# Performance work log

Measured on AMD Instinct MI355X. Metric: run time of the kernel, lower is better.

## Reference

```python
import jax, jax.numpy as jnp
import numpy as np

N_NODES = 100000
N_EDGES = 1600000
D = 128
R = 3
L = 3


def setup_inputs() -> dict:
    key = jax.random.key(0)
    ks = jax.random.split(key, 6)
    features = jax.random.normal(ks[0], (N_NODES, D), dtype=jnp.float32)
    # per-layer relation weights [L, R, D, D], self-loop weights [L, D, D], bias [L, D]
    W = jax.random.normal(ks[1], (L, R, D, D), dtype=jnp.float32) * 0.05
    W_self = jax.random.normal(ks[2], (L, D, D), dtype=jnp.float32) * 0.05
    bias = jnp.zeros((L, D), dtype=jnp.float32)
    src = jax.random.randint(ks[3], (N_EDGES,), 0, N_NODES, dtype=jnp.int32)
    dst = jax.random.randint(ks[4], (N_EDGES,), 0, N_NODES, dtype=jnp.int32)
    etypes = jax.random.randint(ks[5], (N_EDGES,), 0, R, dtype=jnp.int32)
    return {"features": features, "W": W, "W_self": W_self, "bias": bias,
            "src": src, "dst": dst, "etypes": etypes}


def _rel_graph_conv(h, Wl, Wsl, bl, src, dst, etypes):
    # Transform all nodes under every relation once: [N, R, D]
    xW = jnp.einsum('ni,rio->nro', h, Wl)
    # Per-edge message = transformed source feature under edge's relation: [E, D]
    msg = xW[src, etypes]
    # Scatter-add aggregation onto destination nodes
    agg = jax.ops.segment_sum(msg, dst, num_segments=N_NODES)
    # Self-loop + bias (DGL RelGraphConv defaults: self_loop=True, bias=True)
    return agg + h @ Wsl + bl


def reference(features, W, W_self, bias, src, dst, etypes):
    h = features
    for l in range(L):
        h = _rel_graph_conv(h, W[l], W_self[l], bias[l], src, dst, etypes)
    return h
```

## Files before the change

kernel.cpp:

```cpp
#include <hip/hip_runtime.h>


#define DD 128
#define KF 512

typedef __attribute__((ext_vector_type(8))) short short8;
typedef __attribute__((ext_vector_type(4))) float f32x4;

__device__ __forceinline__ float bf2f(ushort u) {
    return __uint_as_float(((unsigned)u) << 16);
}
__device__ __forceinline__ ushort f2bf(float f) {
    unsigned b = __float_as_uint(f);
    return (ushort)((b + 0x7FFFu + ((b >> 16) & 1u)) >> 16);
}
__device__ __forceinline__ void splitbf(float f, ushort& hi, ushort& lo) {
    hi = f2bf(f);
    lo = f2bf(f - bf2f(hi));
}

#define GLOAD_LDS16(g, l)                                                      \
    __builtin_amdgcn_global_load_lds(                                          \
        (const __attribute__((address_space(1))) void*)(g),                    \
        (__attribute__((address_space(3))) void*)(l), 16, 0, 0)

__global__ __launch_bounds__(256) void k_split_feat(
    const float* __restrict__ feat, ushort* __restrict__ h_hi,
    ushort* __restrict__ h_lo, int n4)
{
    int i = blockIdx.x * 256 + threadIdx.x;
    if (i >= n4) return;
    float4 v = reinterpret_cast<const float4*>(feat)[i];
    ushort4 hh, ll;
    splitbf(v.x, hh.x, ll.x); splitbf(v.y, hh.y, ll.y);
    splitbf(v.z, hh.z, ll.z); splitbf(v.w, hh.w, ll.w);
    reinterpret_cast<ushort4*>(h_hi)[i] = hh;
    reinterpret_cast<ushort4*>(h_lo)[i] = ll;
}

__global__ __launch_bounds__(256) void k_build_bimg(
    const float* __restrict__ W, const float* __restrict__ Wself,
    ushort* __restrict__ bh, ushort* __restrict__ bl_)
{
    int idx = blockIdx.x * 256 + threadIdx.x;
    if (idx >= 3 * 65536) return;
    int l = idx >> 16, rem = idx & 65535;
    int j = rem & 7, v = (rem >> 3) & 63, g = (rem >> 9) & 7, c = (rem >> 12) & 15;
    int col = g * 16 + (v & 15);
    int k = c * 32 + ((v >> 4) * 8) + j;
    float val;
    if (k < 128) val = Wself[((size_t)l * 128 + k) * 128 + col];
    else {
        int kk = k - 128, r = kk >> 7, i = kk & 127;
        val = W[(((size_t)l * 3 + r) * 128 + i) * 128 + col];
    }
    ushort hi, lo; splitbf(val, hi, lo);
    bh[idx] = hi; bl_[idx] = lo;
}

__global__ __launch_bounds__(256) void k_zero(int* __restrict__ p, int n) {
    int i = blockIdx.x * 256 + threadIdx.x;
    if (i < n) p[i] = 0;
}
__global__ __launch_bounds__(256) void k_hist3(
    const int* __restrict__ dst, const int* __restrict__ et,
    int* __restrict__ deg, int nEdges) {
    int e = blockIdx.x * 256 + threadIdx.x;
    if (e < nEdges) atomicAdd(&deg[dst[e] * 3 + et[e]], 1);
}
__global__ __launch_bounds__(1024) void k_scanA(
    const int* __restrict__ deg, int* __restrict__ off,
    int* __restrict__ chunkSum, int n) {
    __shared__ int s[1024];
    const int tid = threadIdx.x;
    const int i = blockIdx.x * 1024 + tid;
    int v = (i < n) ? deg[i] : 0;
    s[tid] = v;
    __syncthreads();
    for (int o = 1; o < 1024; o <<= 1) {
        int t = (tid >= o) ? s[tid - o] : 0;
        __syncthreads();
        s[tid] += t;
        __syncthreads();
    }
    if (i < n) off[i] = s[tid] - v;
    if (tid == 1023) chunkSum[blockIdx.x] = s[1023];
}
__global__ __launch_bounds__(512) void k_scanB(int* __restrict__ chunkSum, int nChunks) {
    __shared__ int s[512];
    const int tid = threadIdx.x;
    int v = (tid < nChunks) ? chunkSum[tid] : 0;
    s[tid] = v;
    __syncthreads();
    for (int o = 1; o < 512; o <<= 1) {
        int t = (tid >= o) ? s[tid - o] : 0;
        __syncthreads();
        s[tid] += t;
        __syncthreads();
    }
    if (tid < nChunks) chunkSum[tid] = s[tid] - v;
}
__global__ __launch_bounds__(256) void k_scanC(
    int* __restrict__ off, int* __restrict__ pos,
    const int* __restrict__ chunkBase, int n, int total) {
    int i = blockIdx.x * 256 + threadIdx.x;
    if (i < n) {
        int o = off[i] + chunkBase[i >> 10];
        off[i] = o;
        pos[i] = o;
    }
    if (i == 0) off[n] = total;
}
__global__ __launch_bounds__(256) void k_scatter3(
    const int* __restrict__ src, const int* __restrict__ dst,
    const int* __restrict__ et, int* __restrict__ pos,
    int* __restrict__ csr, int nEdges) {
    int e = blockIdx.x * 256 + threadIdx.x;
    if (e < nEdges) {
        int j = atomicAdd(&pos[dst[e] * 3 + et[e]], 1);
        csr[j] = src[e];
    }
}

__global__ __launch_bounds__(256) void rgcn_gather(
    const ushort* __restrict__ h_hi, const ushort* __restrict__ h_lo,
    const int* __restrict__ off3, const int* __restrict__ csr,
    ushort* __restrict__ aggF_hi, ushort* __restrict__ aggF_lo,
    int nNodes)
{
    const int gtid = blockIdx.x * 256 + threadIdx.x;
    const int gw   = gtid >> 6;
    const int lane = threadIdx.x & 63;
    const int sub  = lane >> 5;
    const int li   = lane & 31;
    const int n    = gw * 2 + sub;
    if (n >= nNodes) return;
    const int e0 = li * 4;

    #pragma unroll
    for (int r = 0; r < 3; ++r) {
        const int b = off3[n * 3 + r];
        const int e = off3[n * 3 + r + 1];
        float ax = 0.f, ay = 0.f, az = 0.f, aw = 0.f;
        int j = b;
        for (; j + 1 < e; j += 2) {
            int s0 = csr[j], s1 = csr[j + 1];
            ushort4 h0 = *reinterpret_cast<const ushort4*>(h_hi + (size_t)s0 * DD + e0);
            ushort4 l0 = *reinterpret_cast<const ushort4*>(h_lo + (size_t)s0 * DD + e0);
            ushort4 h1 = *reinterpret_cast<const ushort4*>(h_hi + (size_t)s1 * DD + e0);
            ushort4 l1 = *reinterpret_cast<const ushort4*>(h_lo + (size_t)s1 * DD + e0);
            ax += (bf2f(h0.x) + bf2f(l0.x)) + (bf2f(h1.x) + bf2f(l1.x));
            ay += (bf2f(h0.y) + bf2f(l0.y)) + (bf2f(h1.y) + bf2f(l1.y));
            az += (bf2f(h0.z) + bf2f(l0.z)) + (bf2f(h1.z) + bf2f(l1.z));
            aw += (bf2f(h0.w) + bf2f(l0.w)) + (bf2f(h1.w) + bf2f(l1.w));
        }
        if (j < e) {
            int s0 = csr[j];
            ushort4 h0 = *reinterpret_cast<const ushort4*>(h_hi + (size_t)s0 * DD + e0);
            ushort4 l0 = *reinterpret_cast<const ushort4*>(h_lo + (size_t)s0 * DD + e0);
            ax += bf2f(h0.x) + bf2f(l0.x);
            ay += bf2f(h0.y) + bf2f(l0.y);
            az += bf2f(h0.z) + bf2f(l0.z);
            aw += bf2f(h0.w) + bf2f(l0.w);
        }
        const size_t o = ((size_t)n * 3 + r) * DD + e0;
        ushort4 hh, ll;
        splitbf(ax, hh.x, ll.x); splitbf(ay, hh.y, ll.y);
        splitbf(az, hh.z, ll.z); splitbf(aw, hh.w, ll.w);
        *reinterpret_cast<ushort4*>(aggF_hi + o) = hh;
        *reinterpret_cast<ushort4*>(aggF_lo + o) = ll;
    }
}

__global__ __launch_bounds__(256) void rgcn_mfma(
    const ushort* __restrict__ h_hi, const ushort* __restrict__ h_lo,
    const ushort* __restrict__ aggF_hi, const ushort* __restrict__ aggF_lo,
    const ushort* __restrict__ bimg_hi, const ushort* __restrict__ bimg_lo,
    const float* __restrict__ bl,
    ushort* __restrict__ out_hi, ushort* __restrict__ out_lo,
    float* __restrict__ out_f32,
    int isFinal, int nNodes)
{
    __shared__ ushort smem[16384];
    ushort* Ah = smem;
    ushort* Al = smem + 4096;
    ushort* Bh = smem + 8192;
    ushort* Bl = smem + 12288;

    const int t = threadIdx.x;
    const int w = t >> 6;
    const int lane = t & 63;
    const int wr = w >> 1, wc = w & 1;
    const int row0 = blockIdx.x * 128;

    f32x4 acc[4][4];
    #pragma unroll
    for (int i = 0; i < 4; ++i)
        #pragma unroll
        for (int jn = 0; jn < 4; ++jn) acc[i][jn] = f32x4{0.f, 0.f, 0.f, 0.f};

    const int arow0 = row0 + (2 * w) * 16 + (lane & 15);
    const int arow1 = row0 + (2 * w + 1) * 16 + (lane & 15);
    const int asub  = (lane >> 4) * 8;

    for (int ch = 0; ch < 16; ++ch) {
        const int kc = ch * 32;
        __syncthreads();
        const ushort* sH; const ushort* sL; size_t stride; int kloc;
        if (kc < 128) { sH = h_hi; sL = h_lo; stride = DD;     kloc = kc; }
        else          { sH = aggF_hi; sL = aggF_lo; stride = 384; kloc = kc - 128; }
        GLOAD_LDS16(sH + (size_t)arow0 * stride + kloc + asub, Ah + (2 * w) * 512);
        GLOAD_LDS16(sH + (size_t)arow1 * stride + kloc + asub, Ah + (2 * w + 1) * 512);
        GLOAD_LDS16(sL + (size_t)arow0 * stride + kloc + asub, Al + (2 * w) * 512);
        GLOAD_LDS16(sL + (size_t)arow1 * stride + kloc + asub, Al + (2 * w + 1) * 512);
        {
            const size_t bbase0 = ((size_t)(ch * 8 + 2 * w) * 64 + lane) * 8;
            const size_t bbase1 = ((size_t)(ch * 8 + 2 * w + 1) * 64 + lane) * 8;
            GLOAD_LDS16(bimg_hi + bbase0, Bh + (2 * w) * 512);
            GLOAD_LDS16(bimg_hi + bbase1, Bh + (2 * w + 1) * 512);
            GLOAD_LDS16(bimg_lo + bbase0, Bl + (2 * w) * 512);
            GLOAD_LDS16(bimg_lo + bbase1, Bl + (2 * w + 1) * 512);
        }
        __syncthreads();

        short8 ah[4], al[4], bh[4], blo[4];
        #pragma unroll
        for (int i = 0; i < 4; ++i) {
            const int mt = wr * 4 + i;
            ah[i]  = *reinterpret_cast<const short8*>(Ah + mt * 512 + lane * 8);
            al[i]  = *reinterpret_cast<const short8*>(Al + mt * 512 + lane * 8);
            const int g = wc * 4 + i;
            bh[i]  = *reinterpret_cast<const short8*>(Bh + g * 512 + lane * 8);
            blo[i] = *reinterpret_cast<const short8*>(Bl + g * 512 + lane * 8);
        }
        #pragma unroll
        for (int i = 0; i < 4; ++i)
            #pragma unroll
            for (int jn = 0; jn < 4; ++jn) {
                acc[i][jn] = __builtin_amdgcn_mfma_f32_16x16x32_bf16(ah[i], bh[jn],  acc[i][jn], 0, 0, 0);
                acc[i][jn] = __builtin_amdgcn_mfma_f32_16x16x32_bf16(ah[i], blo[jn], acc[i][jn], 0, 0, 0);
                acc[i][jn] = __builtin_amdgcn_mfma_f32_16x16x32_bf16(al[i], bh[jn],  acc[i][jn], 0, 0, 0);
                acc[i][jn] = __builtin_amdgcn_mfma_f32_16x16x32_bf16(al[i], blo[jn], acc[i][jn], 0, 0, 0);
            }
    }

    const int colb = wc * 64 + (lane & 15);
    const int rowb = row0 + wr * 64 + (lane >> 4) * 4;
    #pragma unroll
    for (int i = 0; i < 4; ++i) {
        #pragma unroll
        for (int jn = 0; jn < 4; ++jn) {
            const int col = colb + jn * 16;
            const float bb = bl[col];
            #pragma unroll
            for (int rr = 0; rr < 4; ++rr) {
                const int row = rowb + i * 16 + rr;
                if (row < nNodes) {
                    const float v = acc[i][jn][rr] + bb;
                    if (isFinal) {
                        out_f32[(size_t)row * DD + col] = v;
                    } else {
                        ushort hi, lo; splitbf(v, hi, lo);
                        out_hi[(size_t)row * DD + col] = hi;
                        out_lo[(size_t)row * DD + col] = lo;
                    }
                }
            }
        }
    }
}

extern "C" void kernel_launch(void* const* d_in, const int* in_sizes, int n_in,
                              void* d_out, int out_size, void* d_ws, size_t ws_size,
                              hipStream_t stream) {
    const float* feat  = (const float*)d_in[0];
    const float* W     = (const float*)d_in[1];
    const float* Wself = (const float*)d_in[2];
    const float* bias  = (const float*)d_in[3];
    const int*   src   = (const int*)d_in[4];
    const int*   dst   = (const int*)d_in[5];
    const int*   et    = (const int*)d_in[6];
    float* out = (float*)d_out;

    const int nNodes = in_sizes[0] / DD;
    const int nEdges = in_sizes[4];
    const int nBins  = nNodes * 3;

    ushort* h_hi    = (ushort*)d_ws;
    ushort* h_lo    = h_hi + (size_t)nNodes * DD;
    ushort* aggF_hi = h_lo + (size_t)nNodes * DD;
    ushort* aggF_lo = aggF_hi + (size_t)nNodes * 384;
    ushort* bimg_hi = aggF_lo + (size_t)nNodes * 384;
    ushort* bimg_lo = bimg_hi + 3 * 65536;
    int* ip = (int*)(bimg_lo + 3 * 65536);
    int* deg3     = ip;
    int* off3     = deg3 + nBins;
    int* pos3     = off3 + nBins + 1;
    int* chunkSum = pos3 + nBins;
    int* csr      = chunkSum + 512;

    const int nChunks = (nBins + 1023) / 1024;
    const int nEB = (nEdges + 255) / 256;
    const int nBB = (nBins + 255) / 256;

    const int n4 = nNodes * DD / 4;
    k_split_feat<<<(n4 + 255) / 256, 256, 0, stream>>>(feat, h_hi, h_lo, n4);
    k_build_bimg<<<(3 * 65536 + 255) / 256, 256, 0, stream>>>(W, Wself, bimg_hi, bimg_lo);

    k_zero    <<<nBB, 256, 0, stream>>>(deg3, nBins);
    k_hist3   <<<nEB, 256, 0, stream>>>(dst, et, deg3, nEdges);
    k_scanA   <<<nChunks, 1024, 0, stream>>>(deg3, off3, chunkSum, nBins);
    k_scanB   <<<1, 512, 0, stream>>>(chunkSum, nChunks);
    k_scanC   <<<nBB, 256, 0, stream>>>(off3, pos3, chunkSum, nBins, nEdges);
    k_scatter3<<<nEB, 256, 0, stream>>>(src, dst, et, pos3, csr, nEdges);

    const int gatherBlocks = (nNodes + 7) / 8;
    const int gemmBlocks   = (nNodes + 127) / 128;

    for (int l = 0; l < 3; ++l) {
        rgcn_gather<<<gatherBlocks, 256, 0, stream>>>(
            h_hi, h_lo, off3, csr, aggF_hi, aggF_lo, nNodes);
        rgcn_mfma<<<gemmBlocks, 256, 0, stream>>>(
            h_hi, h_lo, aggF_hi, aggF_lo,
            bimg_hi + l * 65536, bimg_lo + l * 65536,
            bias + (size_t)l * DD,
            h_hi, h_lo, out, (l == 2) ? 1 : 0, nNodes);
    }
}
```

Before: 913.4 us.

## Double-buffer A tiles, read weights directly, drop lo*lo MFMA, unroll gather by four

The RGCN MFMA GEMM now double-buffers the A tiles in LDS and prefetches the next K chunk while the current one is computed. B-weight fragments are read straight from global memory into registers instead of being staged through LDS. The al*blo correction MFMA is dropped, cutting matrix work by a quarter at a small precision cost. The aggregation gather loop is unrolled from two edges to four to keep more loads in flight. Risks include a race in the double buffering if the async global-to-LDS loads are not waited on before the barrier, and slightly lower accuracy.

New measurement: 918.2 us. About the same (+0.5%).

```diff
diff --git a/kernel.cpp b/kernel.cpp
--- a/kernel.cpp
+++ b/kernel.cpp
@@ -2,7 +2,6 @@
 
 
 #define DD 128
-#define KF 512
 
 typedef __attribute__((ext_vector_type(8))) short short8;
 typedef __attribute__((ext_vector_type(4))) float f32x4;
@@ -143,18 +142,26 @@
         const int e = off3[n * 3 + r + 1];
         float ax = 0.f, ay = 0.f, az = 0.f, aw = 0.f;
         int j = b;
-        for (; j + 1 < e; j += 2) {
-            int s0 = csr[j], s1 = csr[j + 1];
+        for (; j + 3 < e; j += 4) {
+            int s0 = csr[j], s1 = csr[j + 1], s2 = csr[j + 2], s3 = csr[j + 3];
             ushort4 h0 = *reinterpret_cast<const ushort4*>(h_hi + (size_t)s0 * DD + e0);
             ushort4 l0 = *reinterpret_cast<const ushort4*>(h_lo + (size_t)s0 * DD + e0);
             ushort4 h1 = *reinterpret_cast<const ushort4*>(h_hi + (size_t)s1 * DD + e0);
             ushort4 l1 = *reinterpret_cast<const ushort4*>(h_lo + (size_t)s1 * DD + e0);
-            ax += (bf2f(h0.x) + bf2f(l0.x)) + (bf2f(h1.x) + bf2f(l1.x));
-            ay += (bf2f(h0.y) + bf2f(l0.y)) + (bf2f(h1.y) + bf2f(l1.y));
-            az += (bf2f(h0.z) + bf2f(l0.z)) + (bf2f(h1.z) + bf2f(l1.z));
-            aw += (bf2f(h0.w) + bf2f(l0.w)) + (bf2f(h1.w) + bf2f(l1.w));
-        }
-        if (j < e) {
+            ushort4 h2 = *reinterpret_cast<const ushort4*>(h_hi + (size_t)s2 * DD + e0);
+            ushort4 l2 = *reinterpret_cast<const ushort4*>(h_lo + (size_t)s2 * DD + e0);
+            ushort4 h3 = *reinterpret_cast<const ushort4*>(h_hi + (size_t)s3 * DD + e0);
+            ushort4 l3 = *reinterpret_cast<const ushort4*>(h_lo + (size_t)s3 * DD + e0);
+            ax += (bf2f(h0.x) + bf2f(l0.x)) + (bf2f(h1.x) + bf2f(l1.x))
+                + (bf2f(h2.x) + bf2f(l2.x)) + (bf2f(h3.x) + bf2f(l3.x));
+            ay += (bf2f(h0.y) + bf2f(l0.y)) + (bf2f(h1.y) + bf2f(l1.y))
+                + (bf2f(h2.y) + bf2f(l2.y)) + (bf2f(h3.y) + bf2f(l3.y));
+            az += (bf2f(h0.z) + bf2f(l0.z)) + (bf2f(h1.z) + bf2f(l1.z))
+                + (bf2f(h2.z) + bf2f(l2.z)) + (bf2f(h3.z) + bf2f(l3.z));
+            aw += (bf2f(h0.w) + bf2f(l0.w)) + (bf2f(h1.w) + bf2f(l1.w))
+                + (bf2f(h2.w) + bf2f(l2.w)) + (bf2f(h3.w) + bf2f(l3.w));
+        }
+        for (; j < e; ++j) {
             int s0 = csr[j];
             ushort4 h0 = *reinterpret_cast<const ushort4*>(h_hi + (size_t)s0 * DD + e0);
             ushort4 l0 = *reinterpret_cast<const ushort4*>(h_lo + (size_t)s0 * DD + e0);
@@ -181,11 +188,8 @@
     float* __restrict__ out_f32,
     int isFinal, int nNodes)
 {
-    __shared__ ushort smem[16384];
-    ushort* Ah = smem;
-    ushort* Al = smem + 4096;
-    ushort* Bh = smem + 8192;
-    ushort* Bl = smem + 12288;
+    __shared__ ushort Ah[2][4096];
+    __shared__ ushort Al[2][4096];
 
     const int t = threadIdx.x;
     const int w = t >> 6;
@@ -203,35 +207,38 @@
     const int arow1 = row0 + (2 * w + 1) * 16 + (lane & 15);
     const int asub  = (lane >> 4) * 8;
 
+#define STAGE_A(CH, BUF)                                                          \
+    {                                                                             \
+        const int kc_ = (CH) * 32;                                                \
+        const ushort* sH_; const ushort* sL_; size_t stride_; int kloc_;          \
+        if (kc_ < 128) { sH_ = h_hi; sL_ = h_lo; stride_ = DD;  kloc_ = kc_; }    \
+        else { sH_ = aggF_hi; sL_ = aggF_lo; stride_ = 384; kloc_ = kc_ - 128; }  \
+        GLOAD_LDS16(sH_ + (size_t)arow0 * stride_ + kloc_ + asub, &Ah[BUF][(2 * w) * 512]);     \
+        GLOAD_LDS16(sH_ + (size_t)arow1 * stride_ + kloc_ + asub, &Ah[BUF][(2 * w + 1) * 512]); \
+        GLOAD_LDS16(sL_ + (size_t)arow0 * stride_ + kloc_ + asub, &Al[BUF][(2 * w) * 512]);     \
+        GLOAD_LDS16(sL_ + (size_t)arow1 * stride_ + kloc_ + asub, &Al[BUF][(2 * w + 1) * 512]); \
+    }
+
+    STAGE_A(0, 0);
+    __syncthreads();
+
     for (int ch = 0; ch < 16; ++ch) {
-        const int kc = ch * 32;
-        __syncthreads();
-        const ushort* sH; const ushort* sL; size_t stride; int kloc;
-        if (kc < 128) { sH = h_hi; sL = h_lo; stride = DD;     kloc = kc; }
-        else          { sH = aggF_hi; sL = aggF_lo; stride = 384; kloc = kc - 128; }
-        GLOAD_LDS16(sH + (size_t)arow0 * stride + kloc + asub, Ah + (2 * w) * 512);
-        GLOAD_LDS16(sH + (size_t)arow1 * stride + kloc + asub, Ah + (2 * w + 1) * 512);
-        GLOAD_LDS16(sL + (size_t)arow0 * stride + kloc + asub, Al + (2 * w) * 512);
-        GLOAD_LDS16(sL + (size_t)arow1 * stride + kloc + asub, Al + (2 * w + 1) * 512);
-        {
-            const size_t bbase0 = ((size_t)(ch * 8 + 2 * w) * 64 + lane) * 8;
-            const size_t bbase1 = ((size_t)(ch * 8 + 2 * w + 1) * 64 + lane) * 8;
-            GLOAD_LDS16(bimg_hi + bbase0, Bh + (2 * w) * 512);
-            GLOAD_LDS16(bimg_hi + bbase1, Bh + (2 * w + 1) * 512);
-            GLOAD_LDS16(bimg_lo + bbase0, Bl + (2 * w) * 512);
-            GLOAD_LDS16(bimg_lo + bbase1, Bl + (2 * w + 1) * 512);
-        }
-        __syncthreads();
-
-        short8 ah[4], al[4], bh[4], blo[4];
+        const int cur = ch & 1;
+        if (ch < 15) STAGE_A(ch + 1, cur ^ 1);
+
+        short8 bh[4], blo[4];
+        #pragma unroll
+        for (int jn = 0; jn < 4; ++jn) {
+            const size_t base = ((size_t)(ch * 8 + wc * 4 + jn) * 64 + lane) * 8;
+            bh[jn]  = *reinterpret_cast<const short8*>(bimg_hi + base);
+            blo[jn] = *reinterpret_cast<const short8*>(bimg_lo + base);
+        }
+        short8 ah[4], al[4];
         #pragma unroll
         for (int i = 0; i < 4; ++i) {
             const int mt = wr * 4 + i;
-            ah[i]  = *reinterpret_cast<const short8*>(Ah + mt * 512 + lane * 8);
-            al[i]  = *reinterpret_cast<const short8*>(Al + mt * 512 + lane * 8);
-            const int g = wc * 4 + i;
-            bh[i]  = *reinterpret_cast<const short8*>(Bh + g * 512 + lane * 8);
-            blo[i] = *reinterpret_cast<const short8*>(Bl + g * 512 + lane * 8);
+            ah[i] = *reinterpret_cast<const short8*>(&Ah[cur][mt * 512 + lane * 8]);
+            al[i] = *reinterpret_cast<const short8*>(&Al[cur][mt * 512 + lane * 8]);
         }
         #pragma unroll
         for (int i = 0; i < 4; ++i)
@@ -240,9 +247,10 @@
                 acc[i][jn] = __builtin_amdgcn_mfma_f32_16x16x32_bf16(ah[i], bh[jn],  acc[i][jn], 0, 0, 0);
                 acc[i][jn] = __builtin_amdgcn_mfma_f32_16x16x32_bf16(ah[i], blo[jn], acc[i][jn], 0, 0, 0);
                 acc[i][jn] = __builtin_amdgcn_mfma_f32_16x16x32_bf16(al[i], bh[jn],  acc[i][jn], 0, 0, 0);
-                acc[i][jn] = __builtin_amdgcn_mfma_f32_16x16x32_bf16(al[i], blo[jn], acc[i][jn], 0, 0, 0);
             }
-    }
+        __syncthreads();
+    }
+#undef STAGE_A
 
     const int colb = wc * 64 + (lane & 15);
     const int rowb = row0 + wr * 64 + (lane >> 4) * 4;
```
